# Kernel optimization log

Hardware: AMD Instinct MI355X
Metric: run time of the kernel (lower is better)

## Reference

```python
import jax, jax.numpy as jnp
import numpy as np

B, E, W, HID, HOR = 16, 128, 256, 64, 12
EPS = 1e-5


def conv1d(x, w, b, stride=1, padding=0, groups=1):
    # x: [N, Cin, L], w: [Cout, Cin//groups, K]
    y = jax.lax.conv_general_dilated(x, w, (stride,), [(padding, padding)],
                                     feature_group_count=groups,
                                     dimension_numbers=('NCH', 'OIH', 'NCH'))
    return y + b[None, :, None]


def setup_inputs() -> dict:
    key = jax.random.key(0)
    ks = jax.random.split(key, 20)
    def rn(k, shape, scale):
        return jax.random.normal(k, shape, dtype=jnp.float32) * scale
    return {
        'x': rn(ks[0], (B, 1, W), 1.0),
        'noise': rn(ks[1], (HOR, B * E), 1.0),
        'affine_weight': jnp.ones((E,), jnp.float32),
        'affine_bias': jnp.zeros((E,), jnp.float32),
        'pe_w1': rn(ks[2], (32, 1, 5), 1.0 / np.sqrt(5.0)),
        'pe_b1': jnp.zeros((32,), jnp.float32),
        'bn_gamma': jnp.ones((32,), jnp.float32),
        'bn_beta': jnp.zeros((32,), jnp.float32),
        'bn_mean': jnp.zeros((32,), jnp.float32),
        'bn_var': jnp.ones((32,), jnp.float32),
        'pe_w2': rn(ks[3], (E, 32, 1), 1.0 / np.sqrt(32.0)),
        'pe_b2': jnp.zeros((E,), jnp.float32),
        'net_w1': rn(ks[4], (E, 64, 1, 2), 1.0 / np.sqrt(2.0)),
        'net_b1': jnp.zeros((E, 64), jnp.float32),
        'net_w2': rn(ks[5], (E, 64, 4, 2), 1.0 / np.sqrt(8.0)),
        'net_b2': jnp.zeros((E, 64), jnp.float32),
        'net_w3': rn(ks[6], (E, 1, 64, 1), 1.0 / np.sqrt(64.0)),
        'net_b3': jnp.zeros((E, 1), jnp.float32),
        'gat_wl': rn(ks[7], (HID, HID), 1.0 / np.sqrt(HID)),
        'gat_bl': jnp.zeros((HID,), jnp.float32),
        'gat_wr': rn(ks[8], (HID, HID), 1.0 / np.sqrt(HID)),
        'gat_br': jnp.zeros((HID,), jnp.float32),
        'gat_attn': rn(ks[9], (HID,), 1.0 / np.sqrt(HID)),
        'out_w': rn(ks[10], (E, HID), 1.0 / np.sqrt(HID)),
        'out_b': jnp.zeros((E,), jnp.float32),
        'ce_w': rn(ks[11], (HID, 3), 1.0 / np.sqrt(3.0)),
        'ce_b': jnp.zeros((HID,), jnp.float32),
        'cd_w': rn(ks[12], (4, HID), 1.0 / np.sqrt(HID)),
        'cd_b': jnp.zeros((4,), jnp.float32),
        'q_w': rn(ks[13], (32, W), 1.0 / np.sqrt(W)),
        'q_b': jnp.zeros((32,), jnp.float32),
        'k_w': rn(ks[14], (32, W), 1.0 / np.sqrt(W)),
        'k_b': jnp.zeros((32,), jnp.float32),
    }


def reference(x, noise, affine_weight, affine_bias, pe_w1, pe_b1, bn_gamma, bn_beta,
              bn_mean, bn_var, pe_w2, pe_b2, net_w1, net_b1, net_w2, net_b2, net_w3,
              net_b3, gat_wl, gat_bl, gat_wr, gat_br, gat_attn, out_w, out_b,
              ce_w, ce_b, cd_w, cd_b, q_w, q_b, k_w, k_b):
    # instance norm over time axis (unbiased=False, no eps, as in the torch code)
    mean = jnp.mean(x, axis=2, keepdims=True)              # [B,1,1]
    std = jnp.sqrt(jnp.var(x, axis=2, keepdims=True))
    xn = (x - mean) / std

    # path_encoder: conv(1->32,k5,p2) + ReLU + BN(eval) + conv(32->E,k1)
    h0 = jax.nn.relu(conv1d(xn, pe_w1, pe_b1, padding=2))
    h0 = (h0 - bn_mean[None, :, None]) / jnp.sqrt(bn_var + EPS)[None, :, None]
    h0 = h0 * bn_gamma[None, :, None] + bn_beta[None, :, None]
    xf = conv1d(h0, pe_w2, pe_b2)                          # [B,E,W]
    xf = xf * affine_weight[None, :, None] + affine_bias[None, :, None]

    # adjacency learner: softmax(Q K^T) over nodes, then hard threshold
    q = jnp.einsum('bew,hw->beh', xf, q_w) + q_b           # [B,E,32]
    k = jnp.einsum('bew,hw->beh', xf, k_w) + k_b
    adj_soft = jax.nn.softmax(jnp.einsum('bih,bjh->bij', q, k), axis=-1)  # [B,E,E]
    adj_bin = (adj_soft > 0.5).astype(jnp.float32)

    def cnn1d(xc, w1, b1, w2, b2, w3, b3):
        # xc: [B,1,W] -> [B,1,HID]; kernel=stride=down_factor//2=2
        h1 = jnp.tanh(conv1d(xc, w1, b1, stride=2))
        h2 = jnp.tanh(conv1d(h1, w2, b2, stride=2, groups=16))
        return jnp.tanh(conv1d(h2, w3, b3))

    vcnn = jax.vmap(cnn1d, in_axes=(0, 0, 0, 0, 0, 0, 0))

    def gat(h, adj):
        # GATv2, single head, is_concat: e[b,i,j] = a^T lrelu(g_r[i]+g_l[j])
        gl = jnp.einsum('bnf,of->bno', h, gat_wl) + gat_bl   # [B,N,HID]
        gr = jnp.einsum('bnf,of->bno', h, gat_wr) + gat_br
        gs = gr[:, :, None, :] + gl[:, None, :, :]           # [B,N,N,HID]
        e = jnp.einsum('bijf,f->bij', jax.nn.leaky_relu(gs, 0.2), gat_attn)
        e = jnp.where(adj == 0, jnp.float32(-1e20), e)
        a = jax.nn.softmax(e, axis=2)
        return jnp.einsum('bij,bjf->bif', a, gr)             # [B,N,HID]

    def mech(Q_t, P_t, adj, nz):
        Hh, Ee, Vv = Q_t[:, 0], Q_t[:, 1], Q_t[:, 2]
        al, be, ga, et = P_t[:, 0], P_t[:, 1], P_t[:, 2], P_t[:, 3]
        E_coup = jnp.einsum('bij,bj->bi', adj, Ee.reshape(B, E)).reshape(B * E)
        H_new = Hh - al * Hh
        E_new = Ee + be * Hh - ga * Ee + 0.1 * E_coup
        V_new = Vv + et * Ee + nz * 0.01
        return jnp.stack([H_new, E_new, V_new], axis=1)

    Q0 = jnp.tile(jnp.array([1.0, 0.0, 0.0], jnp.float32), (B * E, 1))

    def step(carry, nz):
        xc, Q_t = carry
        xper = xc.transpose(1, 0, 2)[:, :, None, :]          # [E,B,1,W]
        h = vcnn(xper, net_w1, net_b1, net_w2, net_b2, net_w3, net_b3)
        h = h[:, :, 0, :].transpose(1, 0, 2)                 # [B,E,HID]
        h_temp = gat(h, adj_bin)
        H_causal = jnp.tanh(Q_t @ ce_w.T + ce_b).reshape(B, E, HID)
        h = h + jnp.tanh(h_temp) + H_causal
        x_pred = jnp.einsum('beh,eh->be', h, out_w) + out_b  # grouped conv == per-node dot
        x_new = jnp.concatenate([xc[:, :, 1:], x_pred[:, :, None]], axis=2)
        P_t = jax.nn.sigmoid(h.reshape(B * E, HID) @ cd_w.T + cd_b)
        Q_new = mech(Q_t, P_t, adj_bin, nz)
        return (x_new, Q_new), (x_pred, P_t)

    (_, Q_final), (x_preds, P_all) = jax.lax.scan(step, (xf, Q0), noise)
    x_pred_all = x_preds.transpose(1, 2, 0)                  # [B,E,HOR]
    out = (x_pred_all - affine_bias[None, :, None]) / affine_weight[None, :, None]
    out = out * std + mean
    return out, Q_final.reshape(B, E, 3), P_all[-1].reshape(B, E, 4), adj_soft
```

## Files before the change

kernel.cpp:

```cpp
#include <hip/hip_runtime.h>


typedef __attribute__((ext_vector_type(4))) float f32x4;

struct Params {
  const float *__restrict__ x, *__restrict__ noise, *__restrict__ aw, *__restrict__ ab,
              *__restrict__ pe_w1, *__restrict__ pe_b1, *__restrict__ bn_g, *__restrict__ bn_b,
              *__restrict__ bn_m, *__restrict__ bn_v, *__restrict__ pe_w2, *__restrict__ pe_b2,
              *__restrict__ w1, *__restrict__ b1, *__restrict__ w2, *__restrict__ b2,
              *__restrict__ w3, *__restrict__ b3, *__restrict__ wl, *__restrict__ bl,
              *__restrict__ wr, *__restrict__ br, *__restrict__ attn, *__restrict__ out_w,
              *__restrict__ out_b, *__restrict__ ce_w, *__restrict__ ce_b, *__restrict__ cd_w,
              *__restrict__ cd_b, *__restrict__ q_w, *__restrict__ q_b, *__restrict__ k_w,
              *__restrict__ k_b;
  float* ws;
  float* out;
};

__device__ __forceinline__ float fast_tanh(float x) {
  float t = exp2f(fminf(2.8853900818f * x, 126.0f));
  return 1.0f - 2.0f * __builtin_amdgcn_rcpf(t + 1.0f);
}
__device__ __forceinline__ float fast_sigmoid(float x) {
  float t = exp2f(fminf(-1.44269504f * x, 126.0f));
  return __builtin_amdgcn_rcpf(1.0f + t);
}
__device__ __forceinline__ float wsum(float v) {
  #pragma unroll
  for (int m = 1; m < 64; m <<= 1) v += __shfl_xor(v, m, 64);
  return v;
}
__device__ __forceinline__ float wmax(float v) {
  #pragma unroll
  for (int m = 1; m < 64; m <<= 1) v = fmaxf(v, __shfl_xor(v, m, 64));
  return v;
}
__device__ __forceinline__ float load_llc(const float* p) {
  return __hip_atomic_load(p, __ATOMIC_RELAXED, __HIP_MEMORY_SCOPE_AGENT);
}
__device__ __forceinline__ void store_llc(float* p, float v) {
  __hip_atomic_store(p, v, __ATOMIC_RELAXED, __HIP_MEMORY_SCOPE_AGENT);
}
__device__ __forceinline__ f32x4 load_llc4(const float* p) {
  f32x4 v;
  asm volatile("global_load_dwordx4 %0, %1, off sc0 sc1" : "=v"(v) : "v"(p));
  return v;
}

#define OFF_MS   0
#define OFF_EB   32
#define OFF_CNT  4128
#define OFF_QV   16416
#define OFF_KV   81952
#define OFF_GL   147488
#define OFF_GR   409632
#define OFF_H0   671776
#define OFF_XW   802848
#define OFF_G    1359904
#define OFF_ADJ  1916960

__global__ __launch_bounds__(256)
void k1_h0(Params P) {
  __shared__ float red[8];
  const int tid = threadIdx.x, blk = blockIdx.x;
  const int idx = blk * 256 + tid;
  const int b = idx >> 13, c = (idx >> 8) & 31, w = idx & 255;
  const int lane = tid & 63, wv = tid >> 6;

  float v = P.x[b * 256 + w];
  float s = wsum(v), s2 = wsum(v * v);
  if (lane == 0) { red[wv] = s; red[4 + wv] = s2; }
  __syncthreads();
  float st  = red[0] + red[1] + red[2] + red[3];
  float st2 = red[4] + red[5] + red[6] + red[7];
  float mean = st * (1.f / 256.f);
  float var  = st2 * (1.f / 256.f) - mean * mean;
  float sd   = sqrtf(var);
  float* ms = P.ws + OFF_MS;
  if (tid == 0) { ms[b] = mean; ms[16 + b] = sd; }

  float rstd = 1.f / sd;
  float acc = P.pe_b1[c];
  #pragma unroll
  for (int k = 0; k < 5; k++) {
    int u = w - 2 + k;
    float xv = (u >= 0 && u < 256) ? (P.x[b * 256 + u] - mean) * rstd : 0.f;
    acc += P.pe_w1[c * 5 + k] * xv;
  }
  acc = fmaxf(acc, 0.f);
  float sc = P.bn_g[c] / sqrtf(P.bn_v[c] + 1e-5f);
  (P.ws + OFF_H0)[idx] = (acc - P.bn_m[c]) * sc + P.bn_b[c];
}

__global__ __launch_bounds__(256)
void k2_xf(Params P) {
  const int idx = blockIdx.x * 256 + threadIdx.x;
  const int b = idx >> 15, e = (idx >> 8) & 127, w = idx & 255;
  const float* w2p  = P.pe_w2 + e * 32;
  const float* hcol = P.ws + OFF_H0 + b * 8192 + w;
  float acc = P.pe_b2[e];
  #pragma unroll 8
  for (int c = 0; c < 32; c++) acc += w2p[c] * hcol[c * 256];
  acc = acc * P.aw[e] + P.ab[e];
  (P.ws + OFF_XW)[(b * 128 + e) * 272 + w] = acc;
}

__global__ __launch_bounds__(256)
void k3_G(Params P) {
  const int row = blockIdx.x;
  const int es  = row & 127;
  const int s   = threadIdx.x;
  const float* w1p = P.w1 + es * 128;
  const float* w2p = P.w2 + es * 512;
  const float* w3p = P.w3 + es * 64;
  const float* b1p = P.b1 + es * 64;
  const float* b2p = P.b2 + es * 64;
  const float  b3v = P.b3[es];
  const float* xr  = P.ws + OFF_XW + row * 272;
  if (s >= 253) return;
  float X0 = xr[s], X1 = xr[s + 1], X2 = xr[s + 2], X3 = xr[s + 3];
  float acc = 0.f;
  #pragma unroll 1
  for (int g2 = 0; g2 < 16; g2++) {
    float h1v[8];
    #pragma unroll
    for (int ic = 0; ic < 4; ic++) {
      int ch = g2 * 4 + ic;
      float ww0 = w1p[ch * 2], ww1 = w1p[ch * 2 + 1], bb = b1p[ch];
      h1v[ic * 2 + 0] = fast_tanh(bb + ww0 * X0 + ww1 * X1);
      h1v[ic * 2 + 1] = fast_tanh(bb + ww0 * X2 + ww1 * X3);
    }
    #pragma unroll
    for (int oc = 0; oc < 4; oc++) {
      int ch = g2 * 4 + oc;
      const float* wq = w2p + ch * 8;
      float a2 = b2p[ch];
      #pragma unroll
      for (int u = 0; u < 8; u++) a2 += wq[u] * h1v[u];
      acc += w3p[ch] * fast_tanh(a2);
    }
  }
  (P.ws + OFF_G)[row * 272 + s] = fast_tanh(b3v + acc);
}

__global__ __launch_bounds__(256)
void k4_qk(Params P) {
  const int gtid = blockIdx.x * 256 + threadIdx.x;
  if (gtid < 16) ((int*)(P.ws + OFF_CNT))[gtid * 32] = 0;
  const int half = gtid >> 16;
  const int idx  = gtid & 65535;
  const int row  = idx >> 5, h = idx & 31;
  const float* wm  = half ? P.k_w : P.q_w;
  const float* bv  = half ? P.k_b : P.q_b;
  const float* xr  = P.ws + OFF_XW + row * 272;
  const float* wrw = wm + h * 256;
  float acc = bv[h];
  #pragma unroll 8
  for (int w = 0; w < 256; w += 4) {
    float4 xx = *(const float4*)(xr + w);
    float4 wq = *(const float4*)(wrw + w);
    acc += xx.x * wq.x + xx.y * wq.y + xx.z * wq.z + xx.w * wq.w;
  }
  ((half ? P.ws + OFF_KV : P.ws + OFF_QV))[idx] = acc;
}

__global__ __launch_bounds__(256)
void k5_adj(Params P) {
  __shared__ __align__(16) float hbuf[4 * 64];
  const int tid = threadIdx.x, lane = tid & 63, wv = tid >> 6;
  const int row = blockIdx.x * 4 + wv;
  const int b = row >> 7;
  float* ws = P.ws;
  float* hb = hbuf + wv * 64;
  unsigned char* adjb = (unsigned char*)(ws + OFF_ADJ);

  if (lane < 32) hb[lane] = (ws + OFF_QV)[row * 32 + lane];
  __syncthreads();
  float ev0, ev1;
  #pragma unroll
  for (int half = 0; half < 2; half++) {
    int j = lane + half * 64;
    const float* kr = ws + OFF_KV + (b * 128 + j) * 32;
    float acc = 0.f;
    #pragma unroll
    for (int h = 0; h < 32; h += 4) {
      float4 kk = *(const float4*)(kr + h);
      float4 qq = *(const float4*)(hb + h);
      acc += qq.x * kk.x + qq.y * kk.y + qq.z * kk.z + qq.w * kk.w;
    }
    if (half == 0) ev0 = acc; else ev1 = acc;
  }
  float m   = wmax(fmaxf(ev0, ev1));
  float p0  = __expf(ev0 - m), p1 = __expf(ev1 - m);
  float inv = 1.f / wsum(p0 + p1);
  float a0 = p0 * inv, a1 = p1 * inv;
  P.out[38912 + row * 128 + lane]      = a0;
  P.out[38912 + row * 128 + lane + 64] = a1;
  adjb[row * 128 + lane]      = (a0 > 0.5f) ? 1 : 0;
  adjb[row * 128 + lane + 64] = (a1 > 0.5f) ? 1 : 0;
}

__global__ __launch_bounds__(1024, 4)
void k_scan(Params P) {
  __shared__ __align__(16) float glS_[8192];
  __shared__ __align__(16) float grTS_[8192];
  __shared__ __align__(16) float WlS_[4096];
  __shared__ __align__(16) float WrS_[4096];
  __shared__ __align__(16) float wscb[16 * 336];
  __shared__ __align__(16) float attnS[64];
  const int tid = threadIdx.x, lane = tid & 63, wv = tid >> 6;
  const int row = blockIdx.x * 16 + wv;
  const int b = row >> 7, e = row & 127;
  float* ws = P.ws;
  float* abuf = wscb + wv * 336;
  float* hb   = abuf + 128;
  float* h1b  = abuf + 192;
  float* hist = abuf + 320;
  const float4* hb4   = (const float4*)hb;
  const float4* abuf4 = (const float4*)abuf;
  const float4* attn4 = (const float4*)attnS;
  char* glS  = (char*)glS_;
  char* grTS = (char*)grTS_;
  char* WlSc = (char*)WlS_;
  char* WrSc = (char*)WrS_;
  const float* grow_G = ws + OFF_G + row * 272;
  const unsigned char* arow = (const unsigned char*)(ws + OFF_ADJ) + row * 128;
  int* cntb = (int*)(ws + OFF_CNT) + b * 32;

  {
    int o = tid >> 4, q = tid & 15;
    float4 vl = *(const float4*)(P.wl + o * 64 + q * 4);
    float4 vr = *(const float4*)(P.wr + o * 64 + q * 4);
    int off = o * 256 + ((q ^ (o & 15)) << 4);
    *(float4*)(WlSc + off) = vl;
    *(float4*)(WrSc + off) = vr;
  }
  if (tid < 64) attnS[tid] = P.attn[tid];

  float cew0 = P.ce_w[lane * 3], cew1 = P.ce_w[lane * 3 + 1], cew2 = P.ce_w[lane * 3 + 2];
  float cebv = P.ce_b[lane];
  float cdw0 = P.cd_w[lane], cdw1 = P.cd_w[64 + lane], cdw2 = P.cd_w[128 + lane], cdw3 = P.cd_w[192 + lane];
  float cdb0 = P.cd_b[0], cdb1 = P.cd_b[1], cdb2 = P.cd_b[2], cdb3 = P.cd_b[3];
  float outw = P.out_w[e * 64 + lane], outb = P.out_b[e];
  float blv = P.bl[lane], brv = P.br[lane];
  float awv = P.aw[e], abv = P.ab[e];
  float meanb = ws[OFF_MS + b], stdb = ws[OFF_MS + 16 + b];
  float w10 = P.w1[e * 128 + lane * 2], w11 = P.w1[e * 128 + lane * 2 + 1];
  float b1v = P.b1[e * 64 + lane], b2v = P.b2[e * 64 + lane];
  float w3v = P.w3[e * 64 + lane], b3c = P.b3[e];
  float w2r[8];
  {
    const float4* w24 = (const float4*)(P.w2 + e * 512 + lane * 8);
    float4 a = w24[0], c = w24[1];
    w2r[0] = a.x; w2r[1] = a.y; w2r[2] = a.z; w2r[3] = a.w;
    w2r[4] = c.x; w2r[5] = c.y; w2r[6] = c.z; w2r[7] = c.w;
  }
  const bool a0b = arow[lane] != 0, a1b = arow[lane + 64] != 0;
  float h_own = grow_G[4 * lane];
  float xA = (ws + OFF_XW)[row * 272 + 253];
  float xB = (ws + OFF_XW)[row * 272 + 254];
  float xC = (ws + OFF_XW)[row * 272 + 255];
  float q0 = 1.f, q1 = 0.f, q2 = 0.f;
  if (lane == 0) store_llc(ws + OFF_EB + row, 0.f);

  __syncthreads();

  hb[lane] = h_own;
  __syncthreads();
  float gri;
  {
    float glx = blv, grx = brv;
    const int k = lane & 15;
    #pragma unroll
    for (int q = 0; q < 16; q++) {
      float4 hq  = hb4[q];
      float4 wl4 = *(const float4*)(WlSc + lane * 256 + ((q ^ k) << 4));
      float4 wr4 = *(const float4*)(WrSc + lane * 256 + ((q ^ k) << 4));
      glx += hq.x * wl4.x + hq.y * wl4.y + hq.z * wl4.z + hq.w * wl4.w;
      grx += hq.x * wr4.x + hq.y * wr4.y + hq.z * wr4.z + hq.w * wr4.w;
    }
    store_llc(ws + OFF_GL + row * 64 + lane, glx);
    store_llc(ws + OFF_GR + b * 8192 + lane * 128 + e, grx);
    gri = grx;
  }

  const int jj0 = tid >> 4,          cc0 = tid & 15;
  const int jj1 = (1024 + tid) >> 4, cc1 = tid & 15;
  const int ff0 = tid >> 5,          dd0 = tid & 31;
  const int ff1 = 32 + (tid >> 5),   dd1 = tid & 31;

  #pragma unroll 1
  for (int t = 0; t < 12; t++) {
    asm volatile("s_waitcnt vmcnt(0)" ::: "memory");
    __syncthreads();
    if (tid == 0) {
      __hip_atomic_fetch_add(cntb, 1, __ATOMIC_RELAXED, __HIP_MEMORY_SCOPE_AGENT);
      const int target = (t + 1) * 8;
      while (__hip_atomic_load(cntb, __ATOMIC_RELAXED, __HIP_MEMORY_SCOPE_AGENT) < target)
        __builtin_amdgcn_s_sleep(2);
    }
    __syncthreads();

    const float* glG   = ws + OFF_GL + (t & 1) * 131072 + b * 8192;
    const float* grTG  = ws + OFF_GR + (t & 1) * 131072 + b * 8192;
    const float* EbO   = ws + OFF_EB + (t & 1) * 2048;
    float*       EbN   = ws + OFF_EB + ((t + 1) & 1) * 2048;
    float*       glGn  = ws + OFF_GL + ((t + 1) & 1) * 131072;
    float*       grTGn = ws + OFF_GR + ((t + 1) & 1) * 131072;

    {
      f32x4 vg0 = load_llc4(glG  + jj0 * 64  + cc0 * 4);
      f32x4 vg1 = load_llc4(glG  + jj1 * 64  + cc1 * 4);
      f32x4 vr0 = load_llc4(grTG + ff0 * 128 + dd0 * 4);
      f32x4 vr1 = load_llc4(grTG + ff1 * 128 + dd1 * 4);
      asm volatile("s_waitcnt vmcnt(0)" ::: "memory");
      __builtin_amdgcn_sched_barrier(0);
      *(f32x4*)(glS  + jj0 * 256 + ((cc0 ^ (jj0 & 15)) << 4)) = vg0;
      *(f32x4*)(glS  + jj1 * 256 + ((cc1 ^ (jj1 & 15)) << 4)) = vg1;
      *(f32x4*)(grTS + ff0 * 512 + ((dd0 ^ (ff0 & 15)) << 4)) = vr0;
      *(f32x4*)(grTS + ff1 * 512 + ((dd1 ^ (ff1 & 15)) << 4)) = vr1;
    }
    hb[lane] = gri;
    __syncthreads();

    float ev0 = 0.f, ev1 = 0.f;
    {
      const char* r0 = glS + lane * 256;
      const char* r1 = glS + (lane + 64) * 256;
      const int k = lane & 15;
      #pragma unroll
      for (int c = 0; c < 16; c++) {
        float4 hq = hb4[c];
        float4 aq = attn4[c];
        int off = (c ^ k) << 4;
        float4 g0 = *(const float4*)(r0 + off);
        float4 g1 = *(const float4*)(r1 + off);
        float v;
        v = hq.x + g0.x; ev0 += fmaxf(v, 0.2f * v) * aq.x;
        v = hq.y + g0.y; ev0 += fmaxf(v, 0.2f * v) * aq.y;
        v = hq.z + g0.z; ev0 += fmaxf(v, 0.2f * v) * aq.z;
        v = hq.w + g0.w; ev0 += fmaxf(v, 0.2f * v) * aq.w;
        v = hq.x + g1.x; ev1 += fmaxf(v, 0.2f * v) * aq.x;
        v = hq.y + g1.y; ev1 += fmaxf(v, 0.2f * v) * aq.y;
        v = hq.z + g1.z; ev1 += fmaxf(v, 0.2f * v) * aq.z;
        v = hq.w + g1.w; ev1 += fmaxf(v, 0.2f * v) * aq.w;
      }
    }
    ev0 = a0b ? ev0 : -1e20f;
    ev1 = a1b ? ev1 : -1e20f;
    float m   = wmax(fmaxf(ev0, ev1));
    float p0  = __expf(ev0 - m), p1 = __expf(ev1 - m);
    float inv = 1.f / wsum(p0 + p1);
    abuf[lane]      = p0 * inv;
    abuf[lane + 64] = p1 * inv;
    __syncthreads();

    float ht = 0.f;
    {
      const char* rr = grTS + lane * 512;
      const int k = lane & 15;
      #pragma unroll
      for (int c = 0; c < 32; c++) {
        float4 aq = abuf4[c];
        float4 g  = *(const float4*)(rr + ((c ^ k) << 4));
        ht += aq.x * g.x + aq.y * g.y + aq.z * g.z + aq.w * g.w;
      }
    }

    float hc = fast_tanh(cebv + q0 * cew0 + q1 * cew1 + q2 * cew2);
    float hf = h_own + fast_tanh(ht) + hc;

    float xp = wsum(hf * outw) + outb;
    float d0 = wsum(hf * cdw0);
    float d1 = wsum(hf * cdw1);
    float d2 = wsum(hf * cdw2);
    float d3 = wsum(hf * cdw3);
    float al = fast_sigmoid(d0 + cdb0);
    float be = fast_sigmoid(d1 + cdb1);
    float ga = fast_sigmoid(d2 + cdb2);
    float et = fast_sigmoid(d3 + cdb3);

    float ec = 0.f;
    if (a0b) ec += load_llc(EbO + b * 128 + lane);
    if (a1b) ec += load_llc(EbO + b * 128 + lane + 64);
    ec = wsum(ec);

    float Hn = q0 - al * q0;
    float En = q1 + be * q0 - ga * q1 + 0.1f * ec;
    float Vn = q2 + et * q1 + P.noise[t * 2048 + row] * 0.01f;
    q0 = Hn; q1 = En; q2 = Vn;
    if (lane == 0) {
      store_llc(EbN + row, En);
      P.out[row * 12 + t] = (xp - abv) / awv * stdb + meanb;
      if (t == 11) {
        P.out[24576 + row * 3]     = Hn;
        P.out[24576 + row * 3 + 1] = En;
        P.out[24576 + row * 3 + 2] = Vn;
        P.out[30720 + row * 4]     = al;
        P.out[30720 + row * 4 + 1] = be;
        P.out[30720 + row * 4 + 2] = ga;
        P.out[30720 + row * 4 + 3] = et;
      }
    }

    if (t < 11) {
      float X0 = xA, X1 = xB, X2 = xC, X3 = xp;
      xA = xB; xB = xC; xC = xp;
      float h1a = fast_tanh(b1v + w10 * X0 + w11 * X1);
      float h1c = fast_tanh(b1v + w10 * X2 + w11 * X3);
      h1b[lane * 2]     = h1a;
      h1b[lane * 2 + 1] = h1c;
      __syncthreads();
      const float* h1g = h1b + (lane >> 2) * 8;
      float a2 = b2v;
      #pragma unroll
      for (int u = 0; u < 8; u++) a2 += w2r[u] * h1g[u];
      float h2v = fast_tanh(a2);
      float g3  = wsum(w3v * h2v);
      float Gn  = fast_tanh(b3c + g3);
      if (lane == 0) hist[t] = Gn;

      float hnext;
      if (lane == 63) {
        hnext = Gn;
      } else {
        int gi = (t + 1) + 4 * lane;
        hnext = (gi >= 253) ? hist[gi - 253] : grow_G[gi];
      }
      __syncthreads();
      hb[lane] = hnext;
      __syncthreads();
      float glx = blv, grx = brv;
      const int k = lane & 15;
      #pragma unroll
      for (int q = 0; q < 16; q++) {
        float4 hq  = hb4[q];
        float4 wl4 = *(const float4*)(WlSc + lane * 256 + ((q ^ k) << 4));
        float4 wr4 = *(const float4*)(WrSc + lane * 256 + ((q ^ k) << 4));
        glx += hq.x * wl4.x + hq.y * wl4.y + hq.z * wl4.z + hq.w * wl4.w;
        grx += hq.x * wr4.x + hq.y * wr4.y + hq.z * wr4.z + hq.w * wr4.w;
      }
      store_llc(glGn + row * 64 + lane, glx);
      store_llc(grTGn + b * 8192 + lane * 128 + e, grx);
      gri = grx;
      h_own = hnext;
    }
  }
}

extern "C" void kernel_launch(void* const* d_in, const int* in_sizes, int n_in,
                              void* d_out, int out_size, void* d_ws, size_t ws_size,
                              hipStream_t stream) {
  Params p;
  p.x     = (const float*)d_in[0];  p.noise = (const float*)d_in[1];
  p.aw    = (const float*)d_in[2];  p.ab    = (const float*)d_in[3];
  p.pe_w1 = (const float*)d_in[4];  p.pe_b1 = (const float*)d_in[5];
  p.bn_g  = (const float*)d_in[6];  p.bn_b  = (const float*)d_in[7];
  p.bn_m  = (const float*)d_in[8];  p.bn_v  = (const float*)d_in[9];
  p.pe_w2 = (const float*)d_in[10]; p.pe_b2 = (const float*)d_in[11];
  p.w1    = (const float*)d_in[12]; p.b1    = (const float*)d_in[13];
  p.w2    = (const float*)d_in[14]; p.b2    = (const float*)d_in[15];
  p.w3    = (const float*)d_in[16]; p.b3    = (const float*)d_in[17];
  p.wl    = (const float*)d_in[18]; p.bl    = (const float*)d_in[19];
  p.wr    = (const float*)d_in[20]; p.br    = (const float*)d_in[21];
  p.attn  = (const float*)d_in[22]; p.out_w = (const float*)d_in[23];
  p.out_b = (const float*)d_in[24]; p.ce_w  = (const float*)d_in[25];
  p.ce_b  = (const float*)d_in[26]; p.cd_w  = (const float*)d_in[27];
  p.cd_b  = (const float*)d_in[28]; p.q_w   = (const float*)d_in[29];
  p.q_b   = (const float*)d_in[30]; p.k_w   = (const float*)d_in[31];
  p.k_b   = (const float*)d_in[32];
  p.ws  = (float*)d_ws;
  p.out = (float*)d_out;

  k1_h0<<<dim3(512),  dim3(256), 0, stream>>>(p);
  k2_xf<<<dim3(2048), dim3(256), 0, stream>>>(p);
  k3_G <<<dim3(2048), dim3(256), 0, stream>>>(p);
  k4_qk<<<dim3(512),  dim3(256), 0, stream>>>(p);
  k5_adj<<<dim3(512), dim3(256), 0, stream>>>(p);
  k_scan<<<dim3(128), dim3(1024), 0, stream>>>(p);
}
```

Baseline: 263.4 us.

## Halve scan block size, move GAT weights to global transposed, use wave-local LDS fences

The scan kernel now launches 256 blocks of 512 threads (8 rows each) instead of 128 blocks of 1024, so the per-batch barrier counter waits for 16 arrivals. The Wl/Wr weights are transposed into workspace by k4_qk and read from global/cache inside the matvec, freeing 32KB of LDS per block. Several block-wide __syncthreads that protected only per-wave buffers become wave-local lgkmcnt waits, and the edge-buffer loads are hoisted ahead of the attention phase. The risks are more global traffic for weights, more blocks contending on the cross-block spin barrier, and each block still copying the full gl/gr arrays into LDS, so that staging work is now done twice as often across the grid.

```diff
diff --git a/kernel.cpp b/kernel.cpp
--- a/kernel.cpp
+++ b/kernel.cpp
@@ -46,6 +46,10 @@
   asm volatile("global_load_dwordx4 %0, %1, off sc0 sc1" : "=v"(v) : "v"(p));
   return v;
 }
+__device__ __forceinline__ void lds_fence() {
+  asm volatile("s_waitcnt lgkmcnt(0)" ::: "memory");
+  __builtin_amdgcn_sched_barrier(0);
+}
 
 #define OFF_MS   0
 #define OFF_EB   32
@@ -58,6 +62,8 @@
 #define OFF_XW   802848
 #define OFF_G    1359904
 #define OFF_ADJ  1916960
+#define OFF_WLT  1982496
+#define OFF_WRT  1986592
 
 __global__ __launch_bounds__(256)
 void k1_h0(Params P) {
@@ -147,6 +153,14 @@
 void k4_qk(Params P) {
   const int gtid = blockIdx.x * 256 + threadIdx.x;
   if (gtid < 16) ((int*)(P.ws + OFF_CNT))[gtid * 32] = 0;
+  if (gtid < 4096) {
+    int o = gtid >> 6, f = gtid & 63;
+    (P.ws + OFF_WLT)[f * 64 + o] = P.wl[gtid];
+  } else if (gtid < 8192) {
+    int i = gtid - 4096;
+    int o = i >> 6, f = i & 63;
+    (P.ws + OFF_WRT)[f * 64 + o] = P.wr[i];
+  }
   const int half = gtid >> 16;
   const int idx  = gtid & 65535;
   const int row  = idx >> 5, h = idx & 31;
@@ -200,16 +214,14 @@
   adjb[row * 128 + lane + 64] = (a1 > 0.5f) ? 1 : 0;
 }
 
-__global__ __launch_bounds__(1024, 4)
+__global__ __launch_bounds__(512, 4)
 void k_scan(Params P) {
   __shared__ __align__(16) float glS_[8192];
   __shared__ __align__(16) float grTS_[8192];
-  __shared__ __align__(16) float WlS_[4096];
-  __shared__ __align__(16) float WrS_[4096];
-  __shared__ __align__(16) float wscb[16 * 336];
+  __shared__ __align__(16) float wscb[8 * 336];
   __shared__ __align__(16) float attnS[64];
   const int tid = threadIdx.x, lane = tid & 63, wv = tid >> 6;
-  const int row = blockIdx.x * 16 + wv;
+  const int row = blockIdx.x * 8 + wv;
   const int b = row >> 7, e = row & 127;
   float* ws = P.ws;
   float* abuf = wscb + wv * 336;
@@ -221,20 +233,12 @@
   const float4* attn4 = (const float4*)attnS;
   char* glS  = (char*)glS_;
   char* grTS = (char*)grTS_;
-  char* WlSc = (char*)WlS_;
-  char* WrSc = (char*)WrS_;
   const float* grow_G = ws + OFF_G + row * 272;
   const unsigned char* arow = (const unsigned char*)(ws + OFF_ADJ) + row * 128;
-  int* cntb = (int*)(ws + OFF_CNT) + b * 32;
-
-  {
-    int o = tid >> 4, q = tid & 15;
-    float4 vl = *(const float4*)(P.wl + o * 64 + q * 4);
-    float4 vr = *(const float4*)(P.wr + o * 64 + q * 4);
-    int off = o * 256 + ((q ^ (o & 15)) << 4);
-    *(float4*)(WlSc + off) = vl;
-    *(float4*)(WrSc + off) = vr;
-  }
+  const float* WlT = ws + OFF_WLT;
+  const float* WrT = ws + OFF_WRT;
+  int* cntb = (int*)(ws + OFF_CNT) + (blockIdx.x >> 4) * 32;
+
   if (tid < 64) attnS[tid] = P.attn[tid];
 
   float cew0 = P.ce_w[lane * 3], cew1 = P.ce_w[lane * 3 + 1], cew2 = P.ce_w[lane * 3 + 2];
@@ -266,28 +270,20 @@
   __syncthreads();
 
   hb[lane] = h_own;
-  __syncthreads();
+  lds_fence();
   float gri;
   {
     float glx = blv, grx = brv;
-    const int k = lane & 15;
-    #pragma unroll
-    for (int q = 0; q < 16; q++) {
-      float4 hq  = hb4[q];
-      float4 wl4 = *(const float4*)(WlSc + lane * 256 + ((q ^ k) << 4));
-      float4 wr4 = *(const float4*)(WrSc + lane * 256 + ((q ^ k) << 4));
-      glx += hq.x * wl4.x + hq.y * wl4.y + hq.z * wl4.z + hq.w * wl4.w;
-      grx += hq.x * wr4.x + hq.y * wr4.y + hq.z * wr4.z + hq.w * wr4.w;
+    #pragma unroll 4
+    for (int f = 0; f < 64; f++) {
+      float hv = hb[f];
+      glx += hv * WlT[f * 64 + lane];
+      grx += hv * WrT[f * 64 + lane];
     }
     store_llc(ws + OFF_GL + row * 64 + lane, glx);
     store_llc(ws + OFF_GR + b * 8192 + lane * 128 + e, grx);
     gri = grx;
   }
-
-  const int jj0 = tid >> 4,          cc0 = tid & 15;
-  const int jj1 = (1024 + tid) >> 4, cc1 = tid & 15;
-  const int ff0 = tid >> 5,          dd0 = tid & 31;
-  const int ff1 = 32 + (tid >> 5),   dd1 = tid & 31;
 
   #pragma unroll 1
   for (int t = 0; t < 12; t++) {
@@ -295,7 +291,7 @@
     __syncthreads();
     if (tid == 0) {
       __hip_atomic_fetch_add(cntb, 1, __ATOMIC_RELAXED, __HIP_MEMORY_SCOPE_AGENT);
-      const int target = (t + 1) * 8;
+      const int target = (t + 1) * 16;
       while (__hip_atomic_load(cntb, __ATOMIC_RELAXED, __HIP_MEMORY_SCOPE_AGENT) < target)
         __builtin_amdgcn_s_sleep(2);
     }
@@ -308,17 +304,27 @@
     float*       glGn  = ws + OFF_GL + ((t + 1) & 1) * 131072;
     float*       grTGn = ws + OFF_GR + ((t + 1) & 1) * 131072;
 
+    float ebv0 = load_llc(EbO + b * 128 + lane);
+    float ebv1 = load_llc(EbO + b * 128 + lane + 64);
+
     {
-      f32x4 vg0 = load_llc4(glG  + jj0 * 64  + cc0 * 4);
-      f32x4 vg1 = load_llc4(glG  + jj1 * 64  + cc1 * 4);
-      f32x4 vr0 = load_llc4(grTG + ff0 * 128 + dd0 * 4);
-      f32x4 vr1 = load_llc4(grTG + ff1 * 128 + dd1 * 4);
+      f32x4 vg[4], vr[4];
+      #pragma unroll
+      for (int i = 0; i < 4; i++) {
+        int flat = i * 512 + tid;
+        vg[i] = load_llc4(glG  + (flat >> 4) * 64  + (flat & 15) * 4);
+        vr[i] = load_llc4(grTG + (flat >> 5) * 128 + (flat & 31) * 4);
+      }
       asm volatile("s_waitcnt vmcnt(0)" ::: "memory");
       __builtin_amdgcn_sched_barrier(0);
-      *(f32x4*)(glS  + jj0 * 256 + ((cc0 ^ (jj0 & 15)) << 4)) = vg0;
-      *(f32x4*)(glS  + jj1 * 256 + ((cc1 ^ (jj1 & 15)) << 4)) = vg1;
-      *(f32x4*)(grTS + ff0 * 512 + ((dd0 ^ (ff0 & 15)) << 4)) = vr0;
-      *(f32x4*)(grTS + ff1 * 512 + ((dd1 ^ (ff1 & 15)) << 4)) = vr1;
+      #pragma unroll
+      for (int i = 0; i < 4; i++) {
+        int flat = i * 512 + tid;
+        int j = flat >> 4, c = flat & 15;
+        *(f32x4*)(glS + j * 256 + ((c ^ (j & 15)) << 4)) = vg[i];
+        int f = flat >> 5, d = flat & 31;
+        *(f32x4*)(grTS + f * 512 + ((d ^ (f & 15)) << 4)) = vr[i];
+      }
     }
     hb[lane] = gri;
     __syncthreads();
@@ -353,7 +359,7 @@
     float inv = 1.f / wsum(p0 + p1);
     abuf[lane]      = p0 * inv;
     abuf[lane + 64] = p1 * inv;
-    __syncthreads();
+    lds_fence();
 
     float ht = 0.f;
     {
@@ -380,9 +386,7 @@
     float ga = fast_sigmoid(d2 + cdb2);
     float et = fast_sigmoid(d3 + cdb3);
 
-    float ec = 0.f;
-    if (a0b) ec += load_llc(EbO + b * 128 + lane);
-    if (a1b) ec += load_llc(EbO + b * 128 + lane + 64);
+    float ec = (a0b ? ebv0 : 0.f) + (a1b ? ebv1 : 0.f);
     ec = wsum(ec);
 
     float Hn = q0 - al * q0;
@@ -410,7 +414,7 @@
       float h1c = fast_tanh(b1v + w10 * X2 + w11 * X3);
       h1b[lane * 2]     = h1a;
       h1b[lane * 2 + 1] = h1c;
-      __syncthreads();
+      lds_fence();
       const float* h1g = h1b + (lane >> 2) * 8;
       float a2 = b2v;
       #pragma unroll
@@ -427,18 +431,14 @@
         int gi = (t + 1) + 4 * lane;
         hnext = (gi >= 253) ? hist[gi - 253] : grow_G[gi];
       }
-      __syncthreads();
       hb[lane] = hnext;
-      __syncthreads();
+      lds_fence();
       float glx = blv, grx = brv;
-      const int k = lane & 15;
-      #pragma unroll
-      for (int q = 0; q < 16; q++) {
-        float4 hq  = hb4[q];
-        float4 wl4 = *(const float4*)(WlSc + lane * 256 + ((q ^ k) << 4));
-        float4 wr4 = *(const float4*)(WrSc + lane * 256 + ((q ^ k) << 4));
-        glx += hq.x * wl4.x + hq.y * wl4.y + hq.z * wl4.z + hq.w * wl4.w;
-        grx += hq.x * wr4.x + hq.y * wr4.y + hq.z * wr4.z + hq.w * wr4.w;
+      #pragma unroll 4
+      for (int f = 0; f < 64; f++) {
+        float hv = hb[f];
+        glx += hv * WlT[f * 64 + lane];
+        grx += hv * WrT[f * 64 + lane];
       }
       store_llc(glGn + row * 64 + lane, glx);
       store_llc(grTGn + b * 8192 + lane * 128 + e, grx);
@@ -477,5 +477,5 @@
   k3_G <<<dim3(2048), dim3(256), 0, stream>>>(p);
   k4_qk<<<dim3(512),  dim3(256), 0, stream>>>(p);
   k5_adj<<<dim3(512), dim3(256), 0, stream>>>(p);
-  k_scan<<<dim3(128), dim3(1024), 0, stream>>>(p);
-}
+  k_scan<<<dim3(256), dim3(512), 0, stream>>>(p);
+}
```

Result: slower. 288.0 us (+9.4%).

## Fuse adjacency softmax into scan kernel and replace block barriers with wave-local fences

Applied to the files above, without the earlier changes.

Moves the adjacency softmax from its own k5_adj kernel into the scan kernel's prologue, so one launch and the byte-mask round trip through global memory go away. Block-wide __syncthreads on per-wave LDS buffers become lgkmcnt waits, since those buffers are only touched by one wavefront. The per-step E-buffer loads are issued early alongside the gl/grT tile loads, and the grT tile is written to LDS after the attention-score compute so its load latency overlaps that work. Removing barriers between steps depends on the remaining per-step block barrier to order the shared glS/grTS writes.

```diff
diff --git a/kernel.cpp b/kernel.cpp
--- a/kernel.cpp
+++ b/kernel.cpp
@@ -46,6 +46,15 @@
   asm volatile("global_load_dwordx4 %0, %1, off sc0 sc1" : "=v"(v) : "v"(p));
   return v;
 }
+__device__ __forceinline__ float load_llc1(const float* p) {
+  float v;
+  asm volatile("global_load_dword %0, %1, off sc0 sc1" : "=v"(v) : "v"(p));
+  return v;
+}
+__device__ __forceinline__ void lds_fence() {
+  asm volatile("s_waitcnt lgkmcnt(0)" ::: "memory");
+  __builtin_amdgcn_sched_barrier(0);
+}
 
 #define OFF_MS   0
 #define OFF_EB   32
@@ -57,7 +66,6 @@
 #define OFF_H0   671776
 #define OFF_XW   802848
 #define OFF_G    1359904
-#define OFF_ADJ  1916960
 
 __global__ __launch_bounds__(256)
 void k1_h0(Params P) {
@@ -164,42 +172,6 @@
   ((half ? P.ws + OFF_KV : P.ws + OFF_QV))[idx] = acc;
 }
 
-__global__ __launch_bounds__(256)
-void k5_adj(Params P) {
-  __shared__ __align__(16) float hbuf[4 * 64];
-  const int tid = threadIdx.x, lane = tid & 63, wv = tid >> 6;
-  const int row = blockIdx.x * 4 + wv;
-  const int b = row >> 7;
-  float* ws = P.ws;
-  float* hb = hbuf + wv * 64;
-  unsigned char* adjb = (unsigned char*)(ws + OFF_ADJ);
-
-  if (lane < 32) hb[lane] = (ws + OFF_QV)[row * 32 + lane];
-  __syncthreads();
-  float ev0, ev1;
-  #pragma unroll
-  for (int half = 0; half < 2; half++) {
-    int j = lane + half * 64;
-    const float* kr = ws + OFF_KV + (b * 128 + j) * 32;
-    float acc = 0.f;
-    #pragma unroll
-    for (int h = 0; h < 32; h += 4) {
-      float4 kk = *(const float4*)(kr + h);
-      float4 qq = *(const float4*)(hb + h);
-      acc += qq.x * kk.x + qq.y * kk.y + qq.z * kk.z + qq.w * kk.w;
-    }
-    if (half == 0) ev0 = acc; else ev1 = acc;
-  }
-  float m   = wmax(fmaxf(ev0, ev1));
-  float p0  = __expf(ev0 - m), p1 = __expf(ev1 - m);
-  float inv = 1.f / wsum(p0 + p1);
-  float a0 = p0 * inv, a1 = p1 * inv;
-  P.out[38912 + row * 128 + lane]      = a0;
-  P.out[38912 + row * 128 + lane + 64] = a1;
-  adjb[row * 128 + lane]      = (a0 > 0.5f) ? 1 : 0;
-  adjb[row * 128 + lane + 64] = (a1 > 0.5f) ? 1 : 0;
-}
-
 __global__ __launch_bounds__(1024, 4)
 void k_scan(Params P) {
   __shared__ __align__(16) float glS_[8192];
@@ -224,7 +196,6 @@
   char* WlSc = (char*)WlS_;
   char* WrSc = (char*)WrS_;
   const float* grow_G = ws + OFF_G + row * 272;
-  const unsigned char* arow = (const unsigned char*)(ws + OFF_ADJ) + row * 128;
   int* cntb = (int*)(ws + OFF_CNT) + b * 32;
 
   {
@@ -255,7 +226,34 @@
     w2r[0] = a.x; w2r[1] = a.y; w2r[2] = a.z; w2r[3] = a.w;
     w2r[4] = c.x; w2r[5] = c.y; w2r[6] = c.z; w2r[7] = c.w;
   }
-  const bool a0b = arow[lane] != 0, a1b = arow[lane + 64] != 0;
+
+  bool a0b, a1b;
+  {
+    if (lane < 32) hb[lane] = (ws + OFF_QV)[row * 32 + lane];
+    lds_fence();
+    float e0, e1;
+    #pragma unroll
+    for (int half = 0; half < 2; half++) {
+      int j = lane + half * 64;
+      const float* kr = ws + OFF_KV + (b * 128 + j) * 32;
+      float acc = 0.f;
+      #pragma unroll
+      for (int h = 0; h < 32; h += 4) {
+        float4 kk = *(const float4*)(kr + h);
+        float4 qq = *(const float4*)(hb + h);
+        acc += qq.x * kk.x + qq.y * kk.y + qq.z * kk.z + qq.w * kk.w;
+      }
+      if (half == 0) e0 = acc; else e1 = acc;
+    }
+    float m   = wmax(fmaxf(e0, e1));
+    float p0  = __expf(e0 - m), p1 = __expf(e1 - m);
+    float inv = 1.f / wsum(p0 + p1);
+    float av0 = p0 * inv, av1 = p1 * inv;
+    P.out[38912 + row * 128 + lane]      = av0;
+    P.out[38912 + row * 128 + lane + 64] = av1;
+    a0b = av0 > 0.5f; a1b = av1 > 0.5f;
+  }
+
   float h_own = grow_G[4 * lane];
   float xA = (ws + OFF_XW)[row * 272 + 253];
   float xB = (ws + OFF_XW)[row * 272 + 254];
@@ -266,7 +264,7 @@
   __syncthreads();
 
   hb[lane] = h_own;
-  __syncthreads();
+  lds_fence();
   float gri;
   {
     float glx = blv, grx = brv;
@@ -284,11 +282,6 @@
     gri = grx;
   }
 
-  const int jj0 = tid >> 4,          cc0 = tid & 15;
-  const int jj1 = (1024 + tid) >> 4, cc1 = tid & 15;
-  const int ff0 = tid >> 5,          dd0 = tid & 31;
-  const int ff1 = 32 + (tid >> 5),   dd1 = tid & 31;
-
   #pragma unroll 1
   for (int t = 0; t < 12; t++) {
     asm volatile("s_waitcnt vmcnt(0)" ::: "memory");
@@ -308,20 +301,25 @@
     float*       glGn  = ws + OFF_GL + ((t + 1) & 1) * 131072;
     float*       grTGn = ws + OFF_GR + ((t + 1) & 1) * 131072;
 
-    {
-      f32x4 vg0 = load_llc4(glG  + jj0 * 64  + cc0 * 4);
-      f32x4 vg1 = load_llc4(glG  + jj1 * 64  + cc1 * 4);
-      f32x4 vr0 = load_llc4(grTG + ff0 * 128 + dd0 * 4);
-      f32x4 vr1 = load_llc4(grTG + ff1 * 128 + dd1 * 4);
-      asm volatile("s_waitcnt vmcnt(0)" ::: "memory");
-      __builtin_amdgcn_sched_barrier(0);
-      *(f32x4*)(glS  + jj0 * 256 + ((cc0 ^ (jj0 & 15)) << 4)) = vg0;
-      *(f32x4*)(glS  + jj1 * 256 + ((cc1 ^ (jj1 & 15)) << 4)) = vg1;
-      *(f32x4*)(grTS + ff0 * 512 + ((dd0 ^ (ff0 & 15)) << 4)) = vr0;
-      *(f32x4*)(grTS + ff1 * 512 + ((dd1 ^ (ff1 & 15)) << 4)) = vr1;
-    }
+    float ebv0 = load_llc1(EbO + b * 128 + lane);
+    float ebv1 = load_llc1(EbO + b * 128 + lane + 64);
+    const int jj0 = tid >> 4, cc0 = tid & 15;
+    const int jj1 = 64 + jj0;
+    const int ff0 = tid >> 5, dd0 = tid & 31;
+    const int ff1 = 32 + ff0;
+    f32x4 vg0 = load_llc4(glG  + jj0 * 64  + cc0 * 4);
+    f32x4 vg1 = load_llc4(glG  + jj1 * 64  + cc0 * 4);
+    f32x4 vr0 = load_llc4(grTG + ff0 * 128 + dd0 * 4);
+    f32x4 vr1 = load_llc4(grTG + ff1 * 128 + dd0 * 4);
+
+    asm volatile("s_waitcnt vmcnt(2)" ::: "memory");
+    __builtin_amdgcn_sched_barrier(0);
+    *(f32x4*)(glS + jj0 * 256 + ((cc0 ^ (jj0 & 15)) << 4)) = vg0;
+    *(f32x4*)(glS + jj1 * 256 + ((cc0 ^ (jj1 & 15)) << 4)) = vg1;
     hb[lane] = gri;
-    __syncthreads();
+    asm volatile("s_waitcnt lgkmcnt(0)" ::: "memory");
+    __builtin_amdgcn_sched_barrier(0);
+    __builtin_amdgcn_s_barrier();
 
     float ev0 = 0.f, ev1 = 0.f;
     {
@@ -346,6 +344,12 @@
         v = hq.w + g1.w; ev1 += fmaxf(v, 0.2f * v) * aq.w;
       }
     }
+
+    asm volatile("s_waitcnt vmcnt(0)" ::: "memory");
+    __builtin_amdgcn_sched_barrier(0);
+    *(f32x4*)(grTS + ff0 * 512 + ((dd0 ^ (ff0 & 15)) << 4)) = vr0;
+    *(f32x4*)(grTS + ff1 * 512 + ((dd0 ^ (ff1 & 15)) << 4)) = vr1;
+
     ev0 = a0b ? ev0 : -1e20f;
     ev1 = a1b ? ev1 : -1e20f;
     float m   = wmax(fmaxf(ev0, ev1));
@@ -380,9 +384,7 @@
     float ga = fast_sigmoid(d2 + cdb2);
     float et = fast_sigmoid(d3 + cdb3);
 
-    float ec = 0.f;
-    if (a0b) ec += load_llc(EbO + b * 128 + lane);
-    if (a1b) ec += load_llc(EbO + b * 128 + lane + 64);
+    float ec = (a0b ? ebv0 : 0.f) + (a1b ? ebv1 : 0.f);
     ec = wsum(ec);
 
     float Hn = q0 - al * q0;
@@ -410,7 +412,7 @@
       float h1c = fast_tanh(b1v + w10 * X2 + w11 * X3);
       h1b[lane * 2]     = h1a;
       h1b[lane * 2 + 1] = h1c;
-      __syncthreads();
+      lds_fence();
       const float* h1g = h1b + (lane >> 2) * 8;
       float a2 = b2v;
       #pragma unroll
@@ -427,9 +429,8 @@
         int gi = (t + 1) + 4 * lane;
         hnext = (gi >= 253) ? hist[gi - 253] : grow_G[gi];
       }
-      __syncthreads();
       hb[lane] = hnext;
-      __syncthreads();
+      lds_fence();
       float glx = blv, grx = brv;
       const int k = lane & 15;
       #pragma unroll
@@ -476,6 +477,5 @@
   k2_xf<<<dim3(2048), dim3(256), 0, stream>>>(p);
   k3_G <<<dim3(2048), dim3(256), 0, stream>>>(p);
   k4_qk<<<dim3(512),  dim3(256), 0, stream>>>(p);
-  k5_adj<<<dim3(512), dim3(256), 0, stream>>>(p);
   k_scan<<<dim3(128), dim3(1024), 0, stream>>>(p);
 }
```

Result: slower. 270.2 us (+2.6%).
